# Optimization experiments

Hardware: AMD Instinct MI355X
Metric: run time of the kernel (lower is better)

## Reference

```python
import jax, jax.numpy as jnp
import numpy as np

N = 100000
E = 1600000
IN_CH, H1, H2 = 128, 128, 64


def gcn_conv(x, edge_index, W, b):
    """PyG GCNConv: add self-loops, symmetric normalization, linear + scatter-add."""
    n = x.shape[0]
    row, col = edge_index[0], edge_index[1]
    loop = jnp.arange(n, dtype=edge_index.dtype)
    row = jnp.concatenate([row, loop])  # sources (incl. self loops)
    col = jnp.concatenate([col, loop])  # targets
    h = x @ W                           # [n, out]
    deg = jax.ops.segment_sum(jnp.ones(row.shape[0], dtype=x.dtype), col, num_segments=n)
    dinv = jnp.where(deg > 0, jax.lax.rsqrt(deg), jnp.zeros((), dtype=x.dtype))
    norm = dinv[row] * dinv[col]        # [E+n]
    out = jax.ops.segment_sum(norm[:, None] * h[row], col, num_segments=n)
    return out + b


def setup_inputs() -> dict:
    key = jax.random.key(0)
    ks = jax.random.split(key, 8)
    x = jax.random.normal(ks[0], (N, IN_CH), dtype=jnp.float32)
    edge_index = jax.random.randint(ks[1], (2, E), 0, N, dtype=jnp.int32)
    batch = jnp.zeros((N,), dtype=jnp.int32)
    W1 = jax.random.normal(ks[2], (IN_CH, H1), dtype=jnp.float32) * 0.05
    b1 = jnp.zeros((H1,), dtype=jnp.float32)
    Wmu = jax.random.normal(ks[3], (H1, H2), dtype=jnp.float32) * 0.05
    bmu = jnp.zeros((H2,), dtype=jnp.float32)
    Wls = jax.random.normal(ks[4], (H1, H2), dtype=jnp.float32) * 0.05
    bls = jnp.zeros((H2,), dtype=jnp.float32)
    return {"x": x, "edge_index": edge_index, "batch": batch,
            "W1": W1, "b1": b1, "Wmu": Wmu, "bmu": bmu, "Wls": Wls, "bls": bls}


def reference(x, edge_index, batch, W1, b1, Wmu, bmu, Wls, bls):
    # classifier is None (use_classify=False), dropout=0 -> pure GCN path
    h = jax.nn.relu(gcn_conv(x, edge_index, W1, b1))
    mu = gcn_conv(h, edge_index, Wmu, bmu)
    logstd = gcn_conv(h, edge_index, Wls, bls)
    return (mu, logstd)
```

## Files before the change

### kernel.cpp

```cpp
#include <hip/hip_runtime.h>
#include <hip/hip_bf16.h>


#define BW_SH   9
#define BW      (1 << BW_SH)
#define NBUCK_MAX 256
#define EPB     6144
#define CAP     10240

typedef __attribute__((ext_vector_type(8))) short bf16x8;
typedef __attribute__((ext_vector_type(4))) float f32x4;

__device__ __forceinline__ unsigned bf16rne(float f) {
    unsigned u = __float_as_uint(f);
    return (u + 0x7fffu + ((u >> 16) & 1u)) >> 16;
}
__device__ __forceinline__ float bflo(unsigned u) { return __uint_as_float(u << 16); }
__device__ __forceinline__ float bfhi(unsigned u) { return __uint_as_float(u & 0xffff0000u); }

__global__ void k_init(int* __restrict__ gcur, int nbuck) {
    int t = threadIdx.x;
    for (int b = t; b < nbuck; b += 256) gcur[b] = b * CAP;
}

__global__ void k_wprep(const float* __restrict__ W1,
                        const float* __restrict__ Wmu, const float* __restrict__ Wls,
                        const float* __restrict__ bmu, const float* __restrict__ bls,
                        unsigned short* __restrict__ W1t,
                        unsigned short* __restrict__ Wct,
                        float* __restrict__ bcat) {
    int b = blockIdx.x, t = threadIdx.x;
    if (b < 128) {
        W1t[b * 128 + t] = (unsigned short)bf16rne(W1[t * 128 + b]);
        if (b == 0) bcat[t] = (t < 64) ? bmu[t] : bls[t - 64];
    } else {
        int c = b - 128;
        float w = (c < 64) ? Wmu[t * 64 + c] : Wls[t * 64 + (c - 64)];
        Wct[c * 128 + t] = (unsigned short)bf16rne(w);
    }
}

__global__ __launch_bounds__(256) void k_bucket(
    const int* __restrict__ row, const int* __restrict__ col, int e,
    int* __restrict__ gcur, int* __restrict__ pairs)
{
    __shared__ int items[EPB];
    __shared__ unsigned char bkt[EPB];
    __shared__ int hcnt[NBUCK_MAX];
    __shared__ int lbase[NBUCK_MAX];
    int tid = threadIdx.x;
    int e0 = blockIdx.x * EPB;
    int e1 = min(e, e0 + EPB);
    int m = e1 - e0;
    for (int b = tid; b < NBUCK_MAX; b += 256) hcnt[b] = 0;
    __syncthreads();
    for (int i = tid; i < m; i += 256) {
        int s = row[e0 + i];
        int d = col[e0 + i];
        items[i] = (s << BW_SH) | (d & (BW - 1));
        int b = d >> BW_SH;
        bkt[i] = (unsigned char)b;
        atomicAdd(&hcnt[b], 1);
    }
    __syncthreads();
    for (int b = tid; b < NBUCK_MAX; b += 256)
        lbase[b] = hcnt[b] ? atomicAdd(&gcur[b], hcnt[b]) : 0;
    __syncthreads();
    for (int i = tid; i < m; i += 256) {
        int pos = atomicAdd(&lbase[bkt[i]], 1);
        pairs[pos] = items[i];
    }
}

__global__ __launch_bounds__(256) void k_fill4(
    const int* __restrict__ gcur, const int* __restrict__ pairs,
    int* __restrict__ offs, int* __restrict__ cnt, float* __restrict__ dinv,
    int* __restrict__ esrc, int n)
{
    __shared__ int lcnt[BW];
    __shared__ int loffs[BW];
    __shared__ int lcur[BW];
    __shared__ int sscan[256];
    __shared__ int lesrc[CAP];
    int b = blockIdx.x, tid = threadIdx.x;
    int t0 = b << BW_SH;
    int nt = min(n - t0, BW);
    int base = b * CAP;
    int m = min(gcur[b] - base, CAP);
    for (int i = tid; i < BW; i += 256) lcnt[i] = 0;
    __syncthreads();
    for (int i = tid; i < m; i += 256)
        atomicAdd(&lcnt[pairs[base + i] & (BW - 1)], 1);
    __syncthreads();
    int s = lcnt[2 * tid] + lcnt[2 * tid + 1];
    sscan[tid] = s; __syncthreads();
    for (int d = 1; d < 256; d <<= 1) {
        int u = (tid >= d) ? sscan[tid - d] : 0;
        __syncthreads();
        sscan[tid] += u;
        __syncthreads();
    }
    int ex = sscan[tid] - s;
    loffs[2 * tid] = ex;              lcur[2 * tid] = ex;
    loffs[2 * tid + 1] = ex + lcnt[2 * tid];
    lcur[2 * tid + 1] = ex + lcnt[2 * tid];
    __syncthreads();
    for (int t = tid; t < nt; t += 256) {
        int c = lcnt[t];
        offs[t0 + t] = base + loffs[t];
        cnt[t0 + t]  = c;
        dinv[t0 + t] = 1.0f / sqrtf((float)(c + 1));
    }
    for (int i = tid; i < m; i += 256) {
        int it = pairs[base + i];
        int pos = atomicAdd(&lcur[it & (BW - 1)], 1);
        lesrc[pos] = it >> BW_SH;
    }
    __syncthreads();
    for (int i = tid; i < m; i += 256)
        esrc[base + i] = lesrc[i];
}

__global__ __launch_bounds__(256) void k_prop_bf(
    const unsigned* __restrict__ hbf, const float* __restrict__ dinv,
    const int* __restrict__ offs, const int* __restrict__ cnt,
    const int* __restrict__ esrc,
    unsigned* __restrict__ out_bf,
    const float* __restrict__ bias, int do_relu, int n)
{
    int wid  = (blockIdx.x * blockDim.x + threadIdx.x) >> 6;
    if (wid >= n) return;
    int lane = threadIdx.x & 63;
    int half = lane >> 5;
    int fl   = lane & 31;
    int v = wid;
    float dv = dinv[v];
    int start = offs[v];
    int deg   = cnt[v];
    const uint2* rows = (const uint2*)hbf;

    float a0 = 0.f, a1 = 0.f, a2 = 0.f, a3 = 0.f;
    if (half == 0) {
        uint2 r = rows[(size_t)v * 32 + fl];
        a0 = dv * bflo(r.x); a1 = dv * bfhi(r.x);
        a2 = dv * bflo(r.y); a3 = dv * bfhi(r.y);
    }
    for (int base = 0; base < deg; base += 64) {
        int m = min(64, deg - base);
        int s = 0; float w = 0.f;
        if (lane < m) { s = esrc[start + base + lane]; w = dinv[s]; }
        int j = 0;
        for (; j + 16 <= m; j += 16) {
            int si[8]; float wi[8]; uint2 r[8];
            #pragma unroll
            for (int u = 0; u < 8; ++u) {
                si[u] = __shfl(s, j + 2 * u + half);
                wi[u] = __shfl(w, j + 2 * u + half);
            }
            #pragma unroll
            for (int u = 0; u < 8; ++u) r[u] = rows[(size_t)si[u] * 32 + fl];
            #pragma unroll
            for (int u = 0; u < 8; ++u) {
                a0 = fmaf(wi[u], bflo(r[u].x), a0);
                a1 = fmaf(wi[u], bfhi(r[u].x), a1);
                a2 = fmaf(wi[u], bflo(r[u].y), a2);
                a3 = fmaf(wi[u], bfhi(r[u].y), a3);
            }
        }
        for (; j + 8 <= m; j += 8) {
            int si[4]; float wi[4]; uint2 r[4];
            #pragma unroll
            for (int u = 0; u < 4; ++u) {
                si[u] = __shfl(s, j + 2 * u + half);
                wi[u] = __shfl(w, j + 2 * u + half);
            }
            #pragma unroll
            for (int u = 0; u < 4; ++u) r[u] = rows[(size_t)si[u] * 32 + fl];
            #pragma unroll
            for (int u = 0; u < 4; ++u) {
                a0 = fmaf(wi[u], bflo(r[u].x), a0);
                a1 = fmaf(wi[u], bfhi(r[u].x), a1);
                a2 = fmaf(wi[u], bflo(r[u].y), a2);
                a3 = fmaf(wi[u], bfhi(r[u].y), a3);
            }
        }
        for (; j < m; j += 2) {
            int   ss = __shfl(s, j + half);
            float wv = __shfl(w, j + half);
            uint2 r = rows[(size_t)ss * 32 + fl];
            a0 = fmaf(wv, bflo(r.x), a0); a1 = fmaf(wv, bfhi(r.x), a1);
            a2 = fmaf(wv, bflo(r.y), a2); a3 = fmaf(wv, bfhi(r.y), a3);
        }
    }
    a0 += __shfl_xor(a0, 32);
    a1 += __shfl_xor(a1, 32);
    a2 += __shfl_xor(a2, 32);
    a3 += __shfl_xor(a3, 32);
    if (half == 0) {
        a0 *= dv; a1 *= dv; a2 *= dv; a3 *= dv;
        if (bias) {
            a0 += bias[fl * 4 + 0]; a1 += bias[fl * 4 + 1];
            a2 += bias[fl * 4 + 2]; a3 += bias[fl * 4 + 3];
        }
        if (do_relu) {
            a0 = fmaxf(a0, 0.f); a1 = fmaxf(a1, 0.f);
            a2 = fmaxf(a2, 0.f); a3 = fmaxf(a3, 0.f);
        }
        uint2 pk;
        pk.x = (bf16rne(a1) << 16) | bf16rne(a0);
        pk.y = (bf16rne(a3) << 16) | bf16rne(a2);
        ((uint2*)out_bf)[(size_t)v * 32 + fl] = pk;
    }
}

__global__ __launch_bounds__(256) void k_gemm1(
    const float* __restrict__ X, const unsigned short* __restrict__ W1t,
    unsigned* __restrict__ Hbf, int n)
{
    __shared__ unsigned short ot[4][16][136];
    int tid = threadIdx.x;
    int w = tid >> 6, L = tid & 63;
    int q = L >> 4, ml = L & 15;
    int nb0 = blockIdx.x * 64 + w * 16;
    int node = nb0 + ml;
    bool valid = node < n;
    const bf16x8* Bp = (const bf16x8*)W1t;
    f32x4 acc[8];
    #pragma unroll
    for (int cb = 0; cb < 8; ++cb) { acc[cb][0]=0.f; acc[cb][1]=0.f; acc[cb][2]=0.f; acc[cb][3]=0.f; }
    #pragma unroll
    for (int kc = 0; kc < 4; ++kc) {
        bf16x8 af = {0,0,0,0,0,0,0,0};
        if (valid) {
            const float4* xp = (const float4*)&X[(size_t)node * 128 + kc * 32 + q * 8];
            float4 xa = xp[0], xb = xp[1];
            af[0] = (short)bf16rne(xa.x); af[1] = (short)bf16rne(xa.y);
            af[2] = (short)bf16rne(xa.z); af[3] = (short)bf16rne(xa.w);
            af[4] = (short)bf16rne(xb.x); af[5] = (short)bf16rne(xb.y);
            af[6] = (short)bf16rne(xb.z); af[7] = (short)bf16rne(xb.w);
        }
        #pragma unroll
        for (int cb = 0; cb < 8; ++cb) {
            bf16x8 bfr = Bp[(cb * 16 + ml) * 16 + kc * 4 + q];
            acc[cb] = __builtin_amdgcn_mfma_f32_16x16x32_bf16(af, bfr, acc[cb], 0, 0, 0);
        }
    }
    #pragma unroll
    for (int cb = 0; cb < 8; ++cb)
        #pragma unroll
        for (int r = 0; r < 4; ++r)
            ot[w][q * 4 + r][cb * 16 + ml] = (unsigned short)bf16rne(acc[cb][r]);
    __syncthreads();
    #pragma unroll
    for (int it = 0; it < 4; ++it) {
        int flat = it * 64 + L;
        int row = flat >> 4, cg = flat & 15;
        int nd = nb0 + row;
        if (nd < n) {
            uint4 v = *(const uint4*)&ot[w][row][cg * 8];
            *(uint4*)&Hbf[(size_t)nd * 64 + cg * 4] = v;
        }
    }
}

__global__ __launch_bounds__(256) void k_gemm2(
    const unsigned* __restrict__ Gbf, const unsigned short* __restrict__ Wct,
    const float* __restrict__ bcat, float* __restrict__ out, int n)
{
    __shared__ float ot[4][16][132];
    int tid = threadIdx.x;
    int w = tid >> 6, L = tid & 63;
    int q = L >> 4, ml = L & 15;
    int nb0 = blockIdx.x * 64 + w * 16;
    int node = nb0 + ml;
    bool valid = node < n;
    const bf16x8* Ap = (const bf16x8*)Gbf;
    const bf16x8* Bp = (const bf16x8*)Wct;
    f32x4 acc[8];
    #pragma unroll
    for (int cb = 0; cb < 8; ++cb) { acc[cb][0]=0.f; acc[cb][1]=0.f; acc[cb][2]=0.f; acc[cb][3]=0.f; }
    #pragma unroll
    for (int kc = 0; kc < 4; ++kc) {
        bf16x8 af = {0,0,0,0,0,0,0,0};
        if (valid) af = Ap[(size_t)node * 16 + kc * 4 + q];
        #pragma unroll
        for (int cb = 0; cb < 8; ++cb) {
            bf16x8 bfr = Bp[(cb * 16 + ml) * 16 + kc * 4 + q];
            acc[cb] = __builtin_amdgcn_mfma_f32_16x16x32_bf16(af, bfr, acc[cb], 0, 0, 0);
        }
    }
    #pragma unroll
    for (int cb = 0; cb < 8; ++cb)
        #pragma unroll
        for (int r = 0; r < 4; ++r)
            ot[w][q * 4 + r][cb * 16 + ml] = acc[cb][r];
    __syncthreads();
    #pragma unroll
    for (int it = 0; it < 8; ++it) {
        int flat = it * 64 + L;
        int row = flat >> 5, c4 = flat & 31;
        int col = c4 * 4;
        int nd = nb0 + row;
        if (nd < n) {
            float4 v = *(const float4*)&ot[w][row][col];
            float4 bb = *(const float4*)&bcat[col];
            v.x += bb.x; v.y += bb.y; v.z += bb.z; v.w += bb.w;
            size_t off = (col < 64)
                ? ((size_t)nd * 64 + col)
                : ((size_t)n * 64 + (size_t)nd * 64 + (col - 64));
            *(float4*)&out[off] = v;
        }
    }
}

extern "C" void kernel_launch(void* const* d_in, const int* in_sizes, int n_in,
                              void* d_out, int out_size, void* d_ws, size_t ws_size,
                              hipStream_t stream) {
    const float* x   = (const float*)d_in[0];
    const int*   ei  = (const int*)d_in[1];
    const float* W1  = (const float*)d_in[3];
    const float* b1  = (const float*)d_in[4];
    const float* Wmu = (const float*)d_in[5];
    const float* bmu = (const float*)d_in[6];
    const float* Wls = (const float*)d_in[7];
    const float* bls = (const float*)d_in[8];
    float* out = (float*)d_out;

    int n = in_sizes[0] / 128;
    int e = in_sizes[1] / 2;
    const int* erow = ei;
    const int* ecol = ei + e;
    int nbuck = (n + BW - 1) >> BW_SH;

    char* p = (char*)d_ws;
    auto alloc = [&](size_t bytes) -> char* {
        char* q = p; p += (bytes + 255) & ~(size_t)255; return q;
    };
    int*            gcur  = (int*)           alloc(NBUCK_MAX * 4);
    int*            cnt   = (int*)           alloc((size_t)n * 4);
    int*            offs  = (int*)           alloc((size_t)n * 4);
    float*          dinv  = (float*)         alloc((size_t)n * 4);
    int*            esrc  = (int*)           alloc((size_t)nbuck * CAP * 4);
    unsigned short* W1t   = (unsigned short*)alloc(128 * 128 * 2);
    unsigned short* Wct   = (unsigned short*)alloc(128 * 128 * 2);
    float*          bcat  = (float*)         alloc(128 * 4);
    unsigned*       hbf   = (unsigned*)      alloc((size_t)n * 64 * 4);
    unsigned*       h1bf  = (unsigned*)      alloc((size_t)n * 64 * 4);
    unsigned*       gbf   = (unsigned*)      alloc((size_t)n * 64 * 4);
    int*            pairs = (int*)gbf;

    k_init<<<1, 256, 0, stream>>>(gcur, nbuck);
    k_wprep<<<256, 128, 0, stream>>>(W1, Wmu, Wls, bmu, bls, W1t, Wct, bcat);
    k_bucket<<<(e + EPB - 1) / EPB, 256, 0, stream>>>(erow, ecol, e, gcur, pairs);
    k_fill4<<<nbuck, 256, 0, stream>>>(gcur, pairs, offs, cnt, dinv, esrc, n);

    k_gemm1<<<(n + 63) / 64, 256, 0, stream>>>(x, W1t, hbf, n);
    k_prop_bf<<<(n + 3) / 4, 256, 0, stream>>>(hbf, dinv, offs, cnt, esrc,
                                               h1bf, b1, 1, n);
    k_prop_bf<<<(n + 3) / 4, 256, 0, stream>>>(h1bf, dinv, offs, cnt, esrc,
                                               gbf, nullptr, 0, n);
    k_gemm2<<<(n + 63) / 64, 256, 0, stream>>>(gbf, Wct, bcat, out, n);
}
```

Baseline: 346.3 us.

## Fuse edge bucketing with first GEMM and halve bucket width

Merges the edge-bucketing kernel and the first dense GEMM into one launch, using disjoint block ranges, so the two independent stages run concurrently. Folds the gcur initialization into the weight-prep kernel, which removes one more launch. Halves the bucket width to 256 nodes with 512 buckets and pads the global bucket cursors to separate cache lines to cut atomic contention. In exchange, every block of the fused kernel reserves 40KB of dynamic shared memory, which may lower GEMM occupancy, and the per-bucket capacity of 5120 leaves less headroom.

```diff
diff --git a/kernel.cpp b/kernel.cpp
--- a/kernel.cpp
+++ b/kernel.cpp
@@ -2,11 +2,12 @@
 #include <hip/hip_bf16.h>
 
 
-#define BW_SH   9
+#define BW_SH   8
 #define BW      (1 << BW_SH)
-#define NBUCK_MAX 256
+#define NBUCK_MAX 512
 #define EPB     6144
-#define CAP     10240
+#define CAP     5120
+#define GPAD    16
 
 typedef __attribute__((ext_vector_type(8))) short bf16x8;
 typedef __attribute__((ext_vector_type(4))) float f32x4;
@@ -17,62 +18,111 @@
 }
 __device__ __forceinline__ float bflo(unsigned u) { return __uint_as_float(u << 16); }
 __device__ __forceinline__ float bfhi(unsigned u) { return __uint_as_float(u & 0xffff0000u); }
-
-__global__ void k_init(int* __restrict__ gcur, int nbuck) {
-    int t = threadIdx.x;
-    for (int b = t; b < nbuck; b += 256) gcur[b] = b * CAP;
-}
 
 __global__ void k_wprep(const float* __restrict__ W1,
                         const float* __restrict__ Wmu, const float* __restrict__ Wls,
                         const float* __restrict__ bmu, const float* __restrict__ bls,
                         unsigned short* __restrict__ W1t,
                         unsigned short* __restrict__ Wct,
-                        float* __restrict__ bcat) {
+                        float* __restrict__ bcat,
+                        int* __restrict__ gcur, int nbuck) {
     int b = blockIdx.x, t = threadIdx.x;
     if (b < 128) {
         W1t[b * 128 + t] = (unsigned short)bf16rne(W1[t * 128 + b]);
         if (b == 0) bcat[t] = (t < 64) ? bmu[t] : bls[t - 64];
-    } else {
+    } else if (b < 256) {
         int c = b - 128;
         float w = (c < 64) ? Wmu[t * 64 + c] : Wls[t * 64 + (c - 64)];
         Wct[c * 128 + t] = (unsigned short)bf16rne(w);
-    }
-}
-
-__global__ __launch_bounds__(256) void k_bucket(
+    } else {
+        int idx = (b - 256) * 128 + t;
+        if (idx < nbuck) gcur[idx * GPAD] = idx * CAP;
+    }
+}
+
+__global__ __launch_bounds__(256) void k_bg1(
     const int* __restrict__ row, const int* __restrict__ col, int e,
-    int* __restrict__ gcur, int* __restrict__ pairs)
+    int* __restrict__ gcur, int* __restrict__ pairs,
+    const float* __restrict__ X, const unsigned short* __restrict__ W1t,
+    unsigned* __restrict__ Hbf, int n, int nbb)
 {
-    __shared__ int items[EPB];
-    __shared__ unsigned char bkt[EPB];
-    __shared__ int hcnt[NBUCK_MAX];
-    __shared__ int lbase[NBUCK_MAX];
+    extern __shared__ char dsm[];
     int tid = threadIdx.x;
-    int e0 = blockIdx.x * EPB;
-    int e1 = min(e, e0 + EPB);
-    int m = e1 - e0;
-    for (int b = tid; b < NBUCK_MAX; b += 256) hcnt[b] = 0;
-    __syncthreads();
-    for (int i = tid; i < m; i += 256) {
-        int s = row[e0 + i];
-        int d = col[e0 + i];
-        items[i] = (s << BW_SH) | (d & (BW - 1));
-        int b = d >> BW_SH;
-        bkt[i] = (unsigned char)b;
-        atomicAdd(&hcnt[b], 1);
-    }
-    __syncthreads();
-    for (int b = tid; b < NBUCK_MAX; b += 256)
-        lbase[b] = hcnt[b] ? atomicAdd(&gcur[b], hcnt[b]) : 0;
-    __syncthreads();
-    for (int i = tid; i < m; i += 256) {
-        int pos = atomicAdd(&lbase[bkt[i]], 1);
-        pairs[pos] = items[i];
-    }
-}
-
-__global__ __launch_bounds__(256) void k_fill4(
+    if (blockIdx.x < nbb) {
+        int* items = (int*)dsm;
+        unsigned short* bkt = (unsigned short*)(dsm + 24576);
+        int* hcnt  = (int*)(dsm + 24576 + 12288);
+        int* lbase = hcnt + NBUCK_MAX;
+        int e0 = blockIdx.x * EPB;
+        int e1 = min(e, e0 + EPB);
+        int m = e1 - e0;
+        for (int b = tid; b < NBUCK_MAX; b += 256) hcnt[b] = 0;
+        __syncthreads();
+        for (int i = tid; i < m; i += 256) {
+            int s = row[e0 + i];
+            int d = col[e0 + i];
+            items[i] = (s << BW_SH) | (d & (BW - 1));
+            int b = d >> BW_SH;
+            bkt[i] = (unsigned short)b;
+            atomicAdd(&hcnt[b], 1);
+        }
+        __syncthreads();
+        for (int b = tid; b < NBUCK_MAX; b += 256)
+            lbase[b] = hcnt[b] ? atomicAdd(&gcur[b * GPAD], hcnt[b]) : 0;
+        __syncthreads();
+        for (int i = tid; i < m; i += 256) {
+            int pos = atomicAdd(&lbase[bkt[i]], 1);
+            pairs[pos] = items[i];
+        }
+    } else {
+        unsigned short* ot = (unsigned short*)dsm;
+        int w = tid >> 6, L = tid & 63;
+        int q = L >> 4, ml = L & 15;
+        int nb0 = (blockIdx.x - nbb) * 64 + w * 16;
+        int node = nb0 + ml;
+        bool valid = node < n;
+        const bf16x8* Bp = (const bf16x8*)W1t;
+        f32x4 acc[8];
+        #pragma unroll
+        for (int cb = 0; cb < 8; ++cb) { acc[cb][0]=0.f; acc[cb][1]=0.f; acc[cb][2]=0.f; acc[cb][3]=0.f; }
+        #pragma unroll
+        for (int kc = 0; kc < 4; ++kc) {
+            bf16x8 af = {0,0,0,0,0,0,0,0};
+            if (valid) {
+                const float4* xp = (const float4*)&X[(size_t)node * 128 + kc * 32 + q * 8];
+                float4 xa = xp[0], xb = xp[1];
+                af[0] = (short)bf16rne(xa.x); af[1] = (short)bf16rne(xa.y);
+                af[2] = (short)bf16rne(xa.z); af[3] = (short)bf16rne(xa.w);
+                af[4] = (short)bf16rne(xb.x); af[5] = (short)bf16rne(xb.y);
+                af[6] = (short)bf16rne(xb.z); af[7] = (short)bf16rne(xb.w);
+            }
+            #pragma unroll
+            for (int cb = 0; cb < 8; ++cb) {
+                bf16x8 bfr = Bp[(cb * 16 + ml) * 16 + kc * 4 + q];
+                acc[cb] = __builtin_amdgcn_mfma_f32_16x16x32_bf16(af, bfr, acc[cb], 0, 0, 0);
+            }
+        }
+        #pragma unroll
+        for (int cb = 0; cb < 8; ++cb)
+            #pragma unroll
+            for (int r = 0; r < 4; ++r)
+                ot[(w * 16 + q * 4 + r) * 136 + cb * 16 + ml] =
+                    (unsigned short)bf16rne(acc[cb][r]);
+        __syncthreads();
+        #pragma unroll
+        for (int it = 0; it < 4; ++it) {
+            int flat = it * 64 + L;
+            int rw = flat >> 4, cg = flat & 15;
+            int nd = nb0 + rw;
+            if (nd < n) {
+                uint4 v = *(const uint4*)&ot[(w * 16 + rw) * 136 + cg * 8];
+                *(uint4*)&Hbf[(size_t)nd * 64 + cg * 4] = v;
+            }
+        }
+    }
+}
+
+__global__ __launch_bounds__(256) void k_fill5(
     const int* __restrict__ gcur, const int* __restrict__ pairs,
     int* __restrict__ offs, int* __restrict__ cnt, float* __restrict__ dinv,
     int* __restrict__ esrc, int n)
@@ -86,13 +136,13 @@
     int t0 = b << BW_SH;
     int nt = min(n - t0, BW);
     int base = b * CAP;
-    int m = min(gcur[b] - base, CAP);
-    for (int i = tid; i < BW; i += 256) lcnt[i] = 0;
+    int m = min(gcur[b * GPAD] - base, CAP);
+    lcnt[tid] = 0;
     __syncthreads();
     for (int i = tid; i < m; i += 256)
         atomicAdd(&lcnt[pairs[base + i] & (BW - 1)], 1);
     __syncthreads();
-    int s = lcnt[2 * tid] + lcnt[2 * tid + 1];
+    int s = lcnt[tid];
     sscan[tid] = s; __syncthreads();
     for (int d = 1; d < 256; d <<= 1) {
         int u = (tid >= d) ? sscan[tid - d] : 0;
@@ -101,15 +151,12 @@
         __syncthreads();
     }
     int ex = sscan[tid] - s;
-    loffs[2 * tid] = ex;              lcur[2 * tid] = ex;
-    loffs[2 * tid + 1] = ex + lcnt[2 * tid];
-    lcur[2 * tid + 1] = ex + lcnt[2 * tid];
-    __syncthreads();
-    for (int t = tid; t < nt; t += 256) {
-        int c = lcnt[t];
-        offs[t0 + t] = base + loffs[t];
-        cnt[t0 + t]  = c;
-        dinv[t0 + t] = 1.0f / sqrtf((float)(c + 1));
+    loffs[tid] = ex; lcur[tid] = ex;
+    __syncthreads();
+    if (tid < nt) {
+        offs[t0 + tid] = base + ex;
+        cnt[t0 + tid]  = s;
+        dinv[t0 + tid] = 1.0f / sqrtf((float)(s + 1));
     }
     for (int i = tid; i < m; i += 256) {
         int it = pairs[base + i];
@@ -210,56 +257,6 @@
         pk.x = (bf16rne(a1) << 16) | bf16rne(a0);
         pk.y = (bf16rne(a3) << 16) | bf16rne(a2);
         ((uint2*)out_bf)[(size_t)v * 32 + fl] = pk;
-    }
-}
-
-__global__ __launch_bounds__(256) void k_gemm1(
-    const float* __restrict__ X, const unsigned short* __restrict__ W1t,
-    unsigned* __restrict__ Hbf, int n)
-{
-    __shared__ unsigned short ot[4][16][136];
-    int tid = threadIdx.x;
-    int w = tid >> 6, L = tid & 63;
-    int q = L >> 4, ml = L & 15;
-    int nb0 = blockIdx.x * 64 + w * 16;
-    int node = nb0 + ml;
-    bool valid = node < n;
-    const bf16x8* Bp = (const bf16x8*)W1t;
-    f32x4 acc[8];
-    #pragma unroll
-    for (int cb = 0; cb < 8; ++cb) { acc[cb][0]=0.f; acc[cb][1]=0.f; acc[cb][2]=0.f; acc[cb][3]=0.f; }
-    #pragma unroll
-    for (int kc = 0; kc < 4; ++kc) {
-        bf16x8 af = {0,0,0,0,0,0,0,0};
-        if (valid) {
-            const float4* xp = (const float4*)&X[(size_t)node * 128 + kc * 32 + q * 8];
-            float4 xa = xp[0], xb = xp[1];
-            af[0] = (short)bf16rne(xa.x); af[1] = (short)bf16rne(xa.y);
-            af[2] = (short)bf16rne(xa.z); af[3] = (short)bf16rne(xa.w);
-            af[4] = (short)bf16rne(xb.x); af[5] = (short)bf16rne(xb.y);
-            af[6] = (short)bf16rne(xb.z); af[7] = (short)bf16rne(xb.w);
-        }
-        #pragma unroll
-        for (int cb = 0; cb < 8; ++cb) {
-            bf16x8 bfr = Bp[(cb * 16 + ml) * 16 + kc * 4 + q];
-            acc[cb] = __builtin_amdgcn_mfma_f32_16x16x32_bf16(af, bfr, acc[cb], 0, 0, 0);
-        }
-    }
-    #pragma unroll
-    for (int cb = 0; cb < 8; ++cb)
-        #pragma unroll
-        for (int r = 0; r < 4; ++r)
-            ot[w][q * 4 + r][cb * 16 + ml] = (unsigned short)bf16rne(acc[cb][r]);
-    __syncthreads();
-    #pragma unroll
-    for (int it = 0; it < 4; ++it) {
-        int flat = it * 64 + L;
-        int row = flat >> 4, cg = flat & 15;
-        int nd = nb0 + row;
-        if (nd < n) {
-            uint4 v = *(const uint4*)&ot[w][row][cg * 8];
-            *(uint4*)&Hbf[(size_t)nd * 64 + cg * 4] = v;
-        }
     }
 }
 
@@ -331,12 +328,13 @@
     const int* erow = ei;
     const int* ecol = ei + e;
     int nbuck = (n + BW - 1) >> BW_SH;
+    int nbb   = (e + EPB - 1) / EPB;
 
     char* p = (char*)d_ws;
     auto alloc = [&](size_t bytes) -> char* {
         char* q = p; p += (bytes + 255) & ~(size_t)255; return q;
     };
-    int*            gcur  = (int*)           alloc(NBUCK_MAX * 4);
+    int*            gcur  = (int*)           alloc((size_t)NBUCK_MAX * GPAD * 4);
     int*            cnt   = (int*)           alloc((size_t)n * 4);
     int*            offs  = (int*)           alloc((size_t)n * 4);
     float*          dinv  = (float*)         alloc((size_t)n * 4);
@@ -349,12 +347,12 @@
     unsigned*       gbf   = (unsigned*)      alloc((size_t)n * 64 * 4);
     int*            pairs = (int*)gbf;
 
-    k_init<<<1, 256, 0, stream>>>(gcur, nbuck);
-    k_wprep<<<256, 128, 0, stream>>>(W1, Wmu, Wls, bmu, bls, W1t, Wct, bcat);
-    k_bucket<<<(e + EPB - 1) / EPB, 256, 0, stream>>>(erow, ecol, e, gcur, pairs);
-    k_fill4<<<nbuck, 256, 0, stream>>>(gcur, pairs, offs, cnt, dinv, esrc, n);
-
-    k_gemm1<<<(n + 63) / 64, 256, 0, stream>>>(x, W1t, hbf, n);
+    k_wprep<<<260, 128, 0, stream>>>(W1, Wmu, Wls, bmu, bls, W1t, Wct, bcat,
+                                     gcur, nbuck);
+    k_bg1<<<nbb + (n + 63) / 64, 256, 40960, stream>>>(
+        erow, ecol, e, gcur, pairs, x, W1t, hbf, n, nbb);
+    k_fill5<<<nbuck, 256, 0, stream>>>(gcur, pairs, offs, cnt, dinv, esrc, n);
+
     k_prop_bf<<<(n + 3) / 4, 256, 0, stream>>>(hbf, dinv, offs, cnt, esrc,
                                                h1bf, b1, 1, n);
     k_prop_bf<<<(n + 3) / 4, 256, 0, stream>>>(h1bf, dinv, offs, cnt, esrc,
```

After: 320.3 us. 1.08x faster.
